# Performance work log

Hardware: AMD Instinct MI355X
Metric: run time of the kernel (lower is better)

The kernel has to match this reference:

```python
import jax, jax.numpy as jnp
import numpy as np

N = 50000      # nodes
E = 800000     # edges
D = 128        # in = out features (required by Euler residual update)
GRID_SIZE = 5
K = 3          # spline order
GRID_LO, GRID_HI = -1.0, 1.0
EPSILON = 0.001
NUM_BASES = GRID_SIZE + K  # 8


def make_grid(in_features):
    # extended uniform grid: [in, grid_size + 2k + 1]
    h = (GRID_HI - GRID_LO) / GRID_SIZE
    g = jnp.arange(-K, GRID_SIZE + K + 1, dtype=jnp.float32) * h + GRID_LO
    return jnp.broadcast_to(g, (in_features, g.shape[0]))


def b_splines(x, grid):
    # x: [N, in]; grid: [in, g+2k+1] -> bases: [N, in, g+k] (Cox-de Boor)
    xe = x[..., None]
    bases = ((xe >= grid[:, :-1]) & (xe < grid[:, 1:])).astype(x.dtype)
    for j in range(1, K + 1):
        left = (xe - grid[:, : -(j + 1)]) / (grid[:, j:-1] - grid[:, : -(j + 1)])
        right = (grid[:, j + 1:] - xe) / (grid[:, j + 1:] - grid[:, 1:-j])
        bases = left * bases[..., :-1] + right * bases[..., 1:]
    return bases


def kan_transform(x, base_w, spline_w, grid):
    # efficient-KAN layer (scale_and_bias=False): silu base branch + spline branch
    base = jax.nn.silu(x) @ base_w.T                    # [N, out]
    sb = b_splines(x, grid)                             # [N, in, g+k]
    spl = jnp.einsum('nib,oib->no', sb, spline_w)       # [N, out]
    return base + spl


def gcn_norm_coeffs(edge_index, n):
    # A_hat symmetric normalization: deg includes self-loop (+1)
    src, dst = edge_index[0], edge_index[1]
    deg = jnp.zeros((n,), jnp.float32).at[dst].add(1.0) + 1.0
    dis = jax.lax.rsqrt(deg)
    return dis[src] * dis[dst]


def setup_inputs() -> dict:
    key = jax.random.key(0)
    ks = jax.random.split(key, 6)
    x = jax.random.uniform(ks[0], (N, D), jnp.float32) * 2.0 - 1.0  # in grid_range
    edge_index = jax.random.randint(ks[1], (2, E), 0, N, dtype=jnp.int64)
    base_w_l = jax.random.normal(ks[2], (D, D), jnp.float32) * (1.0 / np.sqrt(D))
    spline_w_l = jax.random.normal(ks[3], (D, D, NUM_BASES), jnp.float32) * 0.1
    base_w_c = jax.random.normal(ks[4], (D, D), jnp.float32) * (1.0 / np.sqrt(D))
    spline_w_c = jax.random.normal(ks[5], (D, D, NUM_BASES), jnp.float32) * 0.1
    return {"x": x, "edge_index": edge_index, "base_w_l": base_w_l,
            "spline_w_l": spline_w_l, "base_w_c": base_w_c,
            "spline_w_c": spline_w_c, "delta_t": 2}


def reference(x, edge_index, base_w_l, spline_w_l, base_w_c, spline_w_c, delta_t):
    grid = make_grid(D)
    src, dst = edge_index[0], edge_index[1]
    norm = gcn_norm_coeffs(edge_index, N)  # [E]

    def layer(h):
        # KANLayer branch on node features
        h_l = kan_transform(h, base_w_l, spline_w_l, grid)
        # KANConv branch: aggregate_first -> normalized scatter-add, then KAN
        msgs = norm[:, None] * h[src]                              # [E, D]
        agg = jax.ops.segment_sum(msgs, dst, num_segments=N)       # [N, D]
        h_c = kan_transform(agg, base_w_c, spline_w_c, grid)
        return h_l + h_c

    for _ in range(int(delta_t)):   # explicit Euler ODE steps
        x = x + EPSILON * layer(x)
    return x
```

## Files before the change

kernel.cpp:

```cpp
#include <hip/hip_runtime.h>
#include <hip/hip_bf16.h>

#define NNODES 50000
#define NEDGES 800000
#define DF 128
#define KW 1152
#define EPS 0.001f
#define XSS 132
#define NB 196

typedef __bf16 bf16x8 __attribute__((ext_vector_type(8)));
typedef __bf16 bf16x4 __attribute__((ext_vector_type(4)));
typedef float  f32x4  __attribute__((ext_vector_type(4)));
typedef unsigned long ulongx2 __attribute__((ext_vector_type(2)));

__global__ void build_wt(const float* __restrict__ bwl, const float* __restrict__ swl,
                         const float* __restrict__ bwc, const float* __restrict__ swc,
                         __bf16* __restrict__ wtl, __bf16* __restrict__ wtc) {
    int gid = blockIdx.x * 256 + threadIdx.x;
    const float* bw = blockIdx.y ? bwc : bwl;
    const float* sw = blockIdx.y ? swc : swl;
    __bf16*      wt = blockIdx.y ? wtc : wtl;
    int o = gid / KW;
    int k = gid - o * KW;
    float v = (k < 128) ? bw[o * DF + k] : sw[o * 1024 + (k - 128)];
    wt[gid] = (__bf16)v;
}

__global__ void cast_x(const float* __restrict__ x, __bf16* __restrict__ xb) {
    int i = blockIdx.x * 256 + threadIdx.x;
    f32x4 a = ((const f32x4*)x)[2 * i];
    f32x4 b = ((const f32x4*)x)[2 * i + 1];
    bf16x8 o;
    o[0] = (__bf16)a[0]; o[1] = (__bf16)a[1]; o[2] = (__bf16)a[2]; o[3] = (__bf16)a[3];
    o[4] = (__bf16)b[0]; o[5] = (__bf16)b[1]; o[6] = (__bf16)b[2]; o[7] = (__bf16)b[3];
    ((bf16x8*)xb)[i] = o;
}

__global__ void deg_count(const int* __restrict__ ei, int* __restrict__ deg) {
    int e = blockIdx.x * 256 + threadIdx.x;
    if (e >= NEDGES) return;
    atomicAdd(&deg[ei[NEDGES + e]], 1);
}

__global__ void scan_part(const int* __restrict__ deg, int* __restrict__ bsum) {
    __shared__ int red[256];
    int t = threadIdx.x;
    int i = blockIdx.x * 256 + t;
    red[t] = (i < NNODES) ? deg[i] : 0;
    __syncthreads();
    for (int off = 128; off > 0; off >>= 1) {
        if (t < off) red[t] += red[t + off];
        __syncthreads();
    }
    if (t == 0) bsum[blockIdx.x] = red[0];
}

__global__ void scan_bsum(const int* __restrict__ bsum, int* __restrict__ boff) {
    __shared__ int buf[256];
    int t = threadIdx.x;
    int v = (t < NB) ? bsum[t] : 0;
    buf[t] = v;
    __syncthreads();
    for (int off = 1; off < 256; off <<= 1) {
        int x = (t >= off) ? buf[t - off] : 0;
        __syncthreads();
        buf[t] += x;
        __syncthreads();
    }
    if (t <= NB) boff[t] = buf[t] - ((t < NB) ? bsum[t] : 0);
}

__global__ void scan_final(const int* __restrict__ deg, const int* __restrict__ boff,
                           int* __restrict__ rowptr) {
    __shared__ int buf[256];
    int t = threadIdx.x;
    int i = blockIdx.x * 256 + t;
    int v = (i < NNODES) ? deg[i] : 0;
    buf[t] = v;
    __syncthreads();
    for (int off = 1; off < 256; off <<= 1) {
        int x = (t >= off) ? buf[t - off] : 0;
        __syncthreads();
        buf[t] += x;
        __syncthreads();
    }
    if (i < NNODES) rowptr[i] = buf[t] - v + boff[blockIdx.x];
    if (blockIdx.x == 0 && t == 0) rowptr[NNODES] = boff[NB];
}

__global__ void fill_csr(const int* __restrict__ ei, const int* __restrict__ deg,
                         const int* __restrict__ rowptr, int* __restrict__ cnt,
                         int* __restrict__ esrc, float* __restrict__ ew) {
    int e = blockIdx.x * 256 + threadIdx.x;
    if (e >= NEDGES) return;
    int s = ei[e];
    int d = ei[NEDGES + e];
    float w = rsqrtf((float)(deg[s] + 1)) * rsqrtf((float)(deg[d] + 1));
    int p = rowptr[d] + atomicAdd(&cnt[d], 1);
    esrc[p] = s;
    ew[p] = w;
}

__global__ __launch_bounds__(256) void agg_gather(
        const int* __restrict__ rowptr, const int* __restrict__ esrc,
        const float* __restrict__ ew, const __bf16* __restrict__ hb,
        __bf16* __restrict__ aggb) {
    const int tid = blockIdx.x * 256 + threadIdx.x;
    const int n = tid >> 5;
    const int l = tid & 31;
    if (n >= NNODES) return;
    int p  = rowptr[n];
    const int pe = rowptr[n + 1];
    f32x4 acc = {0.0f, 0.0f, 0.0f, 0.0f};
    int   cs0, cs1, cs2, cs3;
    float cw0, cw1, cw2, cw3;
    bool have = (p + 3 < pe);
    if (have) {
        cs0 = esrc[p]; cs1 = esrc[p + 1]; cs2 = esrc[p + 2]; cs3 = esrc[p + 3];
        cw0 = ew[p];   cw1 = ew[p + 1];   cw2 = ew[p + 2];   cw3 = ew[p + 3];
    }
    while (have) {
        int np = p + 4;
        bool nh = (np + 3 < pe);
        int   ns0 = 0, ns1 = 0, ns2 = 0, ns3 = 0;
        float nw0 = 0, nw1 = 0, nw2 = 0, nw3 = 0;
        if (nh) {
            ns0 = esrc[np]; ns1 = esrc[np + 1]; ns2 = esrc[np + 2]; ns3 = esrc[np + 3];
            nw0 = ew[np];   nw1 = ew[np + 1];   nw2 = ew[np + 2];   nw3 = ew[np + 3];
        }
        bf16x4 v0 = *(const bf16x4*)(hb + (size_t)cs0 * DF + l * 4);
        bf16x4 v1 = *(const bf16x4*)(hb + (size_t)cs1 * DF + l * 4);
        bf16x4 v2 = *(const bf16x4*)(hb + (size_t)cs2 * DF + l * 4);
        bf16x4 v3 = *(const bf16x4*)(hb + (size_t)cs3 * DF + l * 4);
#pragma unroll
        for (int j = 0; j < 4; ++j)
            acc[j] += cw0 * (float)v0[j] + cw1 * (float)v1[j]
                    + cw2 * (float)v2[j] + cw3 * (float)v3[j];
        p = np;
        cs0 = ns0; cs1 = ns1; cs2 = ns2; cs3 = ns3;
        cw0 = nw0; cw1 = nw1; cw2 = nw2; cw3 = nw3;
        have = nh;
    }
    for (; p < pe; ++p) {
        int   s0 = esrc[p];
        float w0 = ew[p];
        bf16x4 v0 = *(const bf16x4*)(hb + (size_t)s0 * DF + l * 4);
#pragma unroll
        for (int j = 0; j < 4; ++j) acc[j] += w0 * (float)v0[j];
    }
    bf16x4 o;
#pragma unroll
    for (int j = 0; j < 4; ++j) o[j] = (__bf16)acc[j];
    *(bf16x4*)(aggb + (size_t)n * DF + l * 4) = o;
}

__global__ __launch_bounds__(256, 4) void kan_step(
        const float* __restrict__ h,
        const __bf16* __restrict__ xb,
        const __bf16* __restrict__ aggb,
        const __bf16* __restrict__ wtl, const __bf16* __restrict__ wtc,
        float* __restrict__ out, __bf16* __restrict__ outb) {
    __shared__ __bf16 Bs[2][128 * 40];
    __shared__ __bf16 Xs[64 * XSS];

    const int tid  = threadIdx.x;
    const int lane = tid & 63;
    const int w    = tid >> 6;
    const int q    = lane >> 4, l15 = lane & 15;
    const int n0   = blockIdx.x * 64;

    const int so = tid & 127, sh = tid >> 7;
    const int bbase = so * 40 + sh * 16;
    const size_t wrow = (size_t)so * KW + sh * 16;

    const int xrow = tid >> 2, xseg = tid & 3;
    const bool xok = (n0 + xrow) < NNODES;
    const size_t xgoff = (size_t)(n0 + xrow) * DF + xseg * 32;
    const int xloff = xrow * XSS + xseg * 32;

    const int myrow = w * 16 + l15;

    f32x4 acc[8] = {};
    uint4 g0, g1;

    auto stage_x = [&](const __bf16* src) {
        uint4 v0 = {}, v1 = {}, v2 = {}, v3 = {};
        if (xok) {
            const uint4* g = (const uint4*)(src + xgoff);
            v0 = g[0]; v1 = g[1]; v2 = g[2]; v3 = g[3];
        }
        *(uint4*)&Xs[xloff]      = v0;
        *(uint4*)&Xs[xloff + 8]  = v1;
        *(uint4*)&Xs[xloff + 16] = v2;
        *(uint4*)&Xs[xloff + 24] = v3;
    };

    auto loadB = [&](int tn) {
        const __bf16* wtp = (tn >= 36) ? wtc : wtl;
        const int ck = (tn >= 36) ? tn - 36 : tn;
        const uint4* gp = (const uint4*)(wtp + wrow + ck * 32);
        g0 = gp[0]; g1 = gp[1];
    };
    auto writeB = [&](int buf) {
        *(uint4*)&Bs[buf][bbase]     = g0;
        *(uint4*)&Bs[buf][bbase + 8] = g1;
    };

    auto spline_pack = [&](float x) -> bf16x8 {
        float f  = __builtin_fmaf(x, 2.5f, 5.5f);
        float fi = floorf(f);
        int  idx = (int)fi;
        float u  = f - fi;
        float u2 = u * u, u3 = u2 * u;
        float om = 1.0f - u;
        float Wa = u3 * (1.0f / 6.0f);
        float Wb = (((-3.0f * u + 3.0f) * u + 3.0f) * u + 1.0f) * (1.0f / 6.0f);
        float Wc = ((3.0f * u - 6.0f) * u2 + 4.0f) * (1.0f / 6.0f);
        float Wd = om * om * om * (1.0f / 6.0f);
        unsigned long p =
              (unsigned long)__builtin_bit_cast(unsigned short, (__bf16)Wd)
            | ((unsigned long)__builtin_bit_cast(unsigned short, (__bf16)Wc) << 16)
            | ((unsigned long)__builtin_bit_cast(unsigned short, (__bf16)Wb) << 32)
            | ((unsigned long)__builtin_bit_cast(unsigned short, (__bf16)Wa) << 48);
        int tt = idx - 3;
        unsigned long lo, hi;
        if (tt >= 0) {
            int s = (tt & 3) * 16;
            unsigned long sv = p << s;
            unsigned long cr = (p >> (63 - s)) >> 1;
            bool hh = tt >= 4;
            lo = hh ? 0ul : sv;
            hi = hh ? sv : cr;
            if (tt >= 8) { lo = 0; hi = 0; }
        } else {
            int s = (-tt) * 16;
            lo = (tt >= -3) ? (p >> (s & 63)) : 0ul;
            hi = 0;
        }
        ulongx2 r; r[0] = lo; r[1] = hi;
        return __builtin_bit_cast(bf16x8, r);
    };

    auto silu8 = [&](const __bf16* xs) -> bf16x8 {
        bf16x8 v = *(const bf16x8*)xs;
        bf16x8 o;
#pragma unroll
        for (int j = 0; j < 8; ++j) {
            float x = (float)v[j];
            o[j] = (__bf16)(x / (1.0f + __expf(-x)));
        }
        return o;
    };

    stage_x(xb);
    loadB(0); writeB(0);
    __syncthreads();

#pragma unroll 2
    for (int t = 0; t < 72; ++t) {
        const int buf = t & 1;
        const bool more = t + 1 < 72;
        if (more) loadB(t + 1);

        const int ck = (t >= 36) ? t - 36 : t;
        bf16x8 a;
        if (ck < 4) {
            a = silu8(&Xs[myrow * XSS + ck * 32 + q * 8]);
        } else {
            unsigned short u0 = *(const unsigned short*)&Xs[myrow * XSS + (ck - 4) * 4 + q];
            a = spline_pack(__builtin_bit_cast(float, (unsigned)u0 << 16));
        }

        bf16x8 bF[8];
#pragma unroll
        for (int nj = 0; nj < 8; ++nj)
            bF[nj] = *(const bf16x8*)&Bs[buf][(nj * 16 + l15) * 40 + q * 8];
#pragma unroll
        for (int nj = 0; nj < 8; ++nj)
            acc[nj] = __builtin_amdgcn_mfma_f32_16x16x32_bf16(a, bF[nj], acc[nj], 0, 0, 0);

        if (t == 35) {
            __syncthreads();
            stage_x(aggb);
        }
        if (more) writeB(buf ^ 1);
        __syncthreads();
    }

#pragma unroll
    for (int nj = 0; nj < 8; ++nj) {
#pragma unroll
        for (int r = 0; r < 4; ++r) {
            int row = n0 + w * 16 + q * 4 + r;
            int col = nj * 16 + l15;
            if (row < NNODES) {
                size_t idx = (size_t)row * DF + col;
                float v = h[idx] + EPS * acc[nj][r];
                out[idx]  = v;
                outb[idx] = (__bf16)v;
            }
        }
    }
}

extern "C" void kernel_launch(void* const* d_in, const int* in_sizes, int n_in,
                              void* d_out, int out_size, void* d_ws, size_t ws_size,
                              hipStream_t stream) {
    const float* x   = (const float*)d_in[0];
    const int*   ei  = (const int*)d_in[1];
    const float* bwl = (const float*)d_in[2];
    const float* swl = (const float*)d_in[3];
    const float* bwc = (const float*)d_in[4];
    const float* swc = (const float*)d_in[5];
    float* out = (float*)d_out;

    char* ws = (char*)d_ws;
    int*    deg    = (int*)  (ws + 0);
    int*    cnt    = (int*)  (ws + 200000);
    int*    rowptr = (int*)  (ws + 400000);
    int*    bsum   = (int*)  (ws + 600064);
    int*    boff   = (int*)  (ws + 600896);
    int*    esrc   = (int*)  (ws + 601728);
    float*  ew     = (float*)(ws + 3801728);
    __bf16* xb     = (__bf16*)(ws + 7001728);
    __bf16* aggb   = (__bf16*)(ws + 19801728);
    __bf16* wtl    = (__bf16*)(ws + 32601728);
    __bf16* wtc    = (__bf16*)(ws + 32896640);

    build_wt<<<dim3((DF * KW) / 256, 2), 256, 0, stream>>>(bwl, swl, bwc, swc, wtl, wtc);
    cast_x<<<3125, 256, 0, stream>>>(x, xb);

    hipMemsetAsync(deg, 0, 400000, stream);
    deg_count<<<3125, 256, 0, stream>>>(ei, deg);
    scan_part<<<NB, 256, 0, stream>>>(deg, bsum);
    scan_bsum<<<1, 256, 0, stream>>>(bsum, boff);
    scan_final<<<NB, 256, 0, stream>>>(deg, boff, rowptr);
    fill_csr<<<3125, 256, 0, stream>>>(ei, deg, rowptr, cnt, esrc, ew);

    const int gemm_grid = (NNODES + 63) / 64;
    const float* h = x;
    for (int step = 0; step < 2; ++step) {
        agg_gather<<<6250, 256, 0, stream>>>(rowptr, esrc, ew, xb, aggb);
        kan_step<<<gemm_grid, 256, 0, stream>>>(h, xb, aggb, wtl, wtc, out, xb);
        h = out;
    }
}
```

Before: 401.2 us.

## Split node features into 32-wide planes and regroup edge gather per plane

Stores the bf16 node features and aggregates as four feature planes of 32 columns each. The gather kernel runs one grid slice per plane, with 8 lanes per edge processing 8 edges in parallel, and reduces the partial sums with shuffles. Each plane (about 3.2 MB) is small enough to stay cache-resident during the random gathers. Edge source and weight are packed into a single int2 array, and the spline weight bf16 packing now uses a byte-permute instead of four conversions. In exchange, nodes with few edges leave some lanes idle, and the GEMM epilogue writes bf16 output with a strided pattern.

```diff
diff --git a/kernel.cpp b/kernel.cpp
--- a/kernel.cpp
+++ b/kernel.cpp
@@ -8,6 +8,7 @@
 #define EPS 0.001f
 #define XSS 132
 #define NB 196
+#define PSZ (NNODES * 32)
 
 typedef __bf16 bf16x8 __attribute__((ext_vector_type(8)));
 typedef __bf16 bf16x4 __attribute__((ext_vector_type(4)));
@@ -27,14 +28,16 @@
     wt[gid] = (__bf16)v;
 }
 
-__global__ void cast_x(const float* __restrict__ x, __bf16* __restrict__ xb) {
+__global__ void cast_x(const float* __restrict__ x, __bf16* __restrict__ xq) {
     int i = blockIdx.x * 256 + threadIdx.x;
+    int n  = i >> 4;
+    int f0 = (i & 15) * 8;
     f32x4 a = ((const f32x4*)x)[2 * i];
     f32x4 b = ((const f32x4*)x)[2 * i + 1];
     bf16x8 o;
     o[0] = (__bf16)a[0]; o[1] = (__bf16)a[1]; o[2] = (__bf16)a[2]; o[3] = (__bf16)a[3];
     o[4] = (__bf16)b[0]; o[5] = (__bf16)b[1]; o[6] = (__bf16)b[2]; o[7] = (__bf16)b[3];
-    ((bf16x8*)xb)[i] = o;
+    *(bf16x8*)(xq + (size_t)(f0 >> 5) * PSZ + (size_t)n * 32 + (f0 & 31)) = o;
 }
 
 __global__ void deg_count(const int* __restrict__ ei, int* __restrict__ deg) {
@@ -91,76 +94,64 @@
 
 __global__ void fill_csr(const int* __restrict__ ei, const int* __restrict__ deg,
                          const int* __restrict__ rowptr, int* __restrict__ cnt,
-                         int* __restrict__ esrc, float* __restrict__ ew) {
+                         int2* __restrict__ esw) {
     int e = blockIdx.x * 256 + threadIdx.x;
     if (e >= NEDGES) return;
     int s = ei[e];
     int d = ei[NEDGES + e];
     float w = rsqrtf((float)(deg[s] + 1)) * rsqrtf((float)(deg[d] + 1));
     int p = rowptr[d] + atomicAdd(&cnt[d], 1);
-    esrc[p] = s;
-    ew[p] = w;
-}
-
+    esw[p] = make_int2(s, __float_as_int(w));
+}
+
+#define GPW 4
 __global__ __launch_bounds__(256) void agg_gather(
-        const int* __restrict__ rowptr, const int* __restrict__ esrc,
-        const float* __restrict__ ew, const __bf16* __restrict__ hb,
-        __bf16* __restrict__ aggb) {
-    const int tid = blockIdx.x * 256 + threadIdx.x;
-    const int n = tid >> 5;
-    const int l = tid & 31;
-    if (n >= NNODES) return;
-    int p  = rowptr[n];
-    const int pe = rowptr[n + 1];
-    f32x4 acc = {0.0f, 0.0f, 0.0f, 0.0f};
-    int   cs0, cs1, cs2, cs3;
-    float cw0, cw1, cw2, cw3;
-    bool have = (p + 3 < pe);
-    if (have) {
-        cs0 = esrc[p]; cs1 = esrc[p + 1]; cs2 = esrc[p + 2]; cs3 = esrc[p + 3];
-        cw0 = ew[p];   cw1 = ew[p + 1];   cw2 = ew[p + 2];   cw3 = ew[p + 3];
-    }
-    while (have) {
-        int np = p + 4;
-        bool nh = (np + 3 < pe);
-        int   ns0 = 0, ns1 = 0, ns2 = 0, ns3 = 0;
-        float nw0 = 0, nw1 = 0, nw2 = 0, nw3 = 0;
-        if (nh) {
-            ns0 = esrc[np]; ns1 = esrc[np + 1]; ns2 = esrc[np + 2]; ns3 = esrc[np + 3];
-            nw0 = ew[np];   nw1 = ew[np + 1];   nw2 = ew[np + 2];   nw3 = ew[np + 3];
-        }
-        bf16x4 v0 = *(const bf16x4*)(hb + (size_t)cs0 * DF + l * 4);
-        bf16x4 v1 = *(const bf16x4*)(hb + (size_t)cs1 * DF + l * 4);
-        bf16x4 v2 = *(const bf16x4*)(hb + (size_t)cs2 * DF + l * 4);
-        bf16x4 v3 = *(const bf16x4*)(hb + (size_t)cs3 * DF + l * 4);
-#pragma unroll
-        for (int j = 0; j < 4; ++j)
-            acc[j] += cw0 * (float)v0[j] + cw1 * (float)v1[j]
-                    + cw2 * (float)v2[j] + cw3 * (float)v3[j];
-        p = np;
-        cs0 = ns0; cs1 = ns1; cs2 = ns2; cs3 = ns3;
-        cw0 = nw0; cw1 = nw1; cw2 = nw2; cw3 = nw3;
-        have = nh;
-    }
-    for (; p < pe; ++p) {
-        int   s0 = esrc[p];
-        float w0 = ew[p];
-        bf16x4 v0 = *(const bf16x4*)(hb + (size_t)s0 * DF + l * 4);
-#pragma unroll
-        for (int j = 0; j < 4; ++j) acc[j] += w0 * (float)v0[j];
-    }
-    bf16x4 o;
-#pragma unroll
-    for (int j = 0; j < 4; ++j) o[j] = (__bf16)acc[j];
-    *(bf16x4*)(aggb + (size_t)n * DF + l * 4) = o;
+        const int* __restrict__ rowptr, const int2* __restrict__ esw,
+        const __bf16* __restrict__ xq, __bf16* __restrict__ aggq) {
+    const int l    = threadIdx.x & 63;
+    const int wv   = threadIdx.x >> 6;
+    const int slot = l >> 3;
+    const int fo   = (l & 7) * 4;
+    const int pz   = blockIdx.y;
+    const __bf16* xp = xq   + (size_t)pz * PSZ;
+    __bf16*       ap = aggq + (size_t)pz * PSZ;
+    const int nb = (blockIdx.x * 4 + wv) * GPW;
+#pragma unroll
+    for (int g = 0; g < GPW; ++g) {
+        const int n = nb + g;
+        if (n >= NNODES) break;
+        int ps = rowptr[n];
+        const int pe = rowptr[n + 1];
+        f32x4 acc = {0.0f, 0.0f, 0.0f, 0.0f};
+        for (int p0 = ps; p0 < pe; p0 += 8) {
+            int e = p0 + slot;
+            bool valid = e < pe;
+            int2 ev = esw[valid ? e : ps];
+            float w = valid ? __int_as_float(ev.y) : 0.0f;
+            bf16x4 v = *(const bf16x4*)(xp + (size_t)ev.x * 32 + fo);
+#pragma unroll
+            for (int j = 0; j < 4; ++j) acc[j] += w * (float)v[j];
+        }
+#pragma unroll
+        for (int m = 8; m <= 32; m <<= 1) {
+#pragma unroll
+            for (int j = 0; j < 4; ++j) acc[j] += __shfl_xor(acc[j], m, 64);
+        }
+        if (l < 8) {
+            bf16x4 o;
+#pragma unroll
+            for (int j = 0; j < 4; ++j) o[j] = (__bf16)acc[j];
+            *(bf16x4*)(ap + (size_t)n * 32 + l * 4) = o;
+        }
+    }
 }
 
 __global__ __launch_bounds__(256, 4) void kan_step(
         const float* __restrict__ h,
-        const __bf16* __restrict__ xb,
-        const __bf16* __restrict__ aggb,
+        const __bf16* __restrict__ xq,
+        const __bf16* __restrict__ aggq,
         const __bf16* __restrict__ wtl, const __bf16* __restrict__ wtc,
-        float* __restrict__ out, __bf16* __restrict__ outb) {
+        float* __restrict__ out, __bf16* __restrict__ outq) {
     __shared__ __bf16 Bs[2][128 * 40];
     __shared__ __bf16 Xs[64 * XSS];
 
@@ -176,7 +167,7 @@
 
     const int xrow = tid >> 2, xseg = tid & 3;
     const bool xok = (n0 + xrow) < NNODES;
-    const size_t xgoff = (size_t)(n0 + xrow) * DF + xseg * 32;
+    const size_t xgoff = (size_t)xseg * PSZ + (size_t)(n0 + xrow) * 32;
     const int xloff = xrow * XSS + xseg * 32;
 
     const int myrow = w * 16 + l15;
@@ -218,11 +209,11 @@
         float Wb = (((-3.0f * u + 3.0f) * u + 3.0f) * u + 1.0f) * (1.0f / 6.0f);
         float Wc = ((3.0f * u - 6.0f) * u2 + 4.0f) * (1.0f / 6.0f);
         float Wd = om * om * om * (1.0f / 6.0f);
-        unsigned long p =
-              (unsigned long)__builtin_bit_cast(unsigned short, (__bf16)Wd)
-            | ((unsigned long)__builtin_bit_cast(unsigned short, (__bf16)Wc) << 16)
-            | ((unsigned long)__builtin_bit_cast(unsigned short, (__bf16)Wb) << 32)
-            | ((unsigned long)__builtin_bit_cast(unsigned short, (__bf16)Wa) << 48);
+        unsigned lo32 = __builtin_amdgcn_perm(__builtin_bit_cast(unsigned, Wc),
+                                              __builtin_bit_cast(unsigned, Wd), 0x07060302u);
+        unsigned hi32 = __builtin_amdgcn_perm(__builtin_bit_cast(unsigned, Wa),
+                                              __builtin_bit_cast(unsigned, Wb), 0x07060302u);
+        unsigned long p = (unsigned long)lo32 | ((unsigned long)hi32 << 32);
         int tt = idx - 3;
         unsigned long lo, hi;
         if (tt >= 0) {
@@ -253,7 +244,7 @@
         return o;
     };
 
-    stage_x(xb);
+    stage_x(xq);
     loadB(0); writeB(0);
     __syncthreads();
 
@@ -282,7 +273,7 @@
 
         if (t == 35) {
             __syncthreads();
-            stage_x(aggb);
+            stage_x(aggq);
         }
         if (more) writeB(buf ^ 1);
         __syncthreads();
@@ -297,8 +288,8 @@
             if (row < NNODES) {
                 size_t idx = (size_t)row * DF + col;
                 float v = h[idx] + EPS * acc[nj][r];
-                out[idx]  = v;
-                outb[idx] = (__bf16)v;
+                out[idx] = v;
+                outq[(size_t)(col >> 5) * PSZ + (size_t)row * 32 + (col & 31)] = (__bf16)v;
             }
         }
     }
@@ -321,28 +312,27 @@
     int*    rowptr = (int*)  (ws + 400000);
     int*    bsum   = (int*)  (ws + 600064);
     int*    boff   = (int*)  (ws + 600896);
-    int*    esrc   = (int*)  (ws + 601728);
-    float*  ew     = (float*)(ws + 3801728);
-    __bf16* xb     = (__bf16*)(ws + 7001728);
-    __bf16* aggb   = (__bf16*)(ws + 19801728);
+    int2*   esw    = (int2*) (ws + 601728);
+    __bf16* xq     = (__bf16*)(ws + 7001728);
+    __bf16* aggq   = (__bf16*)(ws + 19801728);
     __bf16* wtl    = (__bf16*)(ws + 32601728);
     __bf16* wtc    = (__bf16*)(ws + 32896640);
 
     build_wt<<<dim3((DF * KW) / 256, 2), 256, 0, stream>>>(bwl, swl, bwc, swc, wtl, wtc);
-    cast_x<<<3125, 256, 0, stream>>>(x, xb);
+    cast_x<<<3125, 256, 0, stream>>>(x, xq);
 
     hipMemsetAsync(deg, 0, 400000, stream);
     deg_count<<<3125, 256, 0, stream>>>(ei, deg);
     scan_part<<<NB, 256, 0, stream>>>(deg, bsum);
     scan_bsum<<<1, 256, 0, stream>>>(bsum, boff);
     scan_final<<<NB, 256, 0, stream>>>(deg, boff, rowptr);
-    fill_csr<<<3125, 256, 0, stream>>>(ei, deg, rowptr, cnt, esrc, ew);
+    fill_csr<<<3125, 256, 0, stream>>>(ei, deg, rowptr, cnt, esw);
 
     const int gemm_grid = (NNODES + 63) / 64;
     const float* h = x;
     for (int step = 0; step < 2; ++step) {
-        agg_gather<<<6250, 256, 0, stream>>>(rowptr, esrc, ew, xb, aggb);
-        kan_step<<<gemm_grid, 256, 0, stream>>>(h, xb, aggb, wtl, wtc, out, xb);
+        agg_gather<<<dim3(3125, 4), 256, 0, stream>>>(rowptr, esw, xq, aggq);
+        kan_step<<<gemm_grid, 256, 0, stream>>>(h, xq, aggq, wtl, wtc, out, xq);
         h = out;
     }
 }
```

Measured after the change: 468.5 us. +16.8%, slower.
